# Optimization experiments

Measured on AMD Instinct MI355X. Metric: run time of the kernel, lower is better.

The kernel has to match this reference:

```python
import jax, jax.numpy as jnp
import numpy as np
from jax import lax

EPS = 1e-4
THRESHOLD = 0.0


@jax.custom_vjp
def ternary(x):
    return jnp.where(x <= -THRESHOLD, -1.0,
                     jnp.where(x >= THRESHOLD, 1.0, 0.0)).astype(x.dtype)


def _ternary_fwd(x):
    return ternary(x), x


def _ternary_bwd(x, g):
    # STE: pass gradient where -1 < x < 1, zero where |x| >= 1
    mask = (x < 1.0) & (x > -1.0)
    return (g * mask.astype(g.dtype),)


ternary.defvjp(_ternary_fwd, _ternary_bwd)


def setup_inputs() -> dict:
    key = jax.random.key(0)
    k1, k2, k3 = jax.random.split(key, 3)
    N, C_in, H, W = 32, 256, 56, 56
    C_out, K = 256, 3
    x = jax.random.normal(k1, (N, C_in, H, W), dtype=jnp.float32)
    gamma = jnp.ones((C_in,), dtype=jnp.float32)
    beta = jnp.zeros((C_in,), dtype=jnp.float32)
    fan_in = C_in * K * K
    weight = jax.random.normal(k2, (C_out, C_in, K, K), dtype=jnp.float32) / np.sqrt(fan_in)
    bias = jax.random.normal(k3, (C_out,), dtype=jnp.float32) * 0.01
    return {"x": x, "gamma": gamma, "beta": beta, "weight": weight, "bias": bias}


def reference(x, gamma, beta, weight, bias):
    # BatchNorm2d (training mode: batch statistics, biased var), eps=1e-4
    mean = jnp.mean(x, axis=(0, 2, 3), keepdims=True)
    var = jnp.mean(jnp.square(x - mean), axis=(0, 2, 3), keepdims=True)
    xn = (x - mean) * lax.rsqrt(var + EPS)
    xn = xn * gamma[None, :, None, None] + beta[None, :, None, None]
    # Ternarize to {-1, 0, 1}
    t = ternary(xn)
    # Conv2d stride=1, padding=1 (NCHW / OIHW)
    y = lax.conv_general_dilated(
        t, weight, window_strides=(1, 1), padding=[(1, 1), (1, 1)],
        dimension_numbers=("NCHW", "OIHW", "NCHW"))
    y = y + bias[None, :, None, None]
    return jax.nn.relu(y)
```

## Files before the change

### kernel.cpp

```cpp
#include <hip/hip_runtime.h>
#include <stdint.h>

#define NN 32
#define CI 256
#define CO 256
#define HH 56
#define WW 56
#define TPH 58
#define TPW 72
#define CNT (NN*HH*WW)

typedef int i32x4 __attribute__((ext_vector_type(4)));

__device__ __forceinline__ void gld16(const void* g, void* l) {
    __builtin_amdgcn_global_load_lds(
        (const __attribute__((address_space(1))) void*)(uintptr_t)g,
        (__attribute__((address_space(3))) void*)(uint32_t)(uintptr_t)l,
        16, 0, 0);
}

__global__ void stats_part(const float* __restrict__ x, double* __restrict__ part) {
    const int c = blockIdx.x, sp = blockIdx.y;
    double s = 0.0, ss = 0.0;
    const size_t base = ((size_t)(sp * 4) * CI + c) * 3136;
    for (int idx = threadIdx.x; idx < 4 * 784; idx += 256) {
        int nl = idx / 784, q = idx % 784;
        const float4 v = *(const float4*)(x + base + (size_t)nl * CI * 3136 + q * 4);
        double a = v.x, b = v.y, cc = v.z, d = v.w;
        s  += (a + b) + (cc + d);
        ss += (a * a + b * b) + (cc * cc + d * d);
    }
    for (int off = 32; off > 0; off >>= 1) {
        s  += __shfl_down(s, off, 64);
        ss += __shfl_down(ss, off, 64);
    }
    __shared__ double red[8];
    int wid = threadIdx.x >> 6, lane = threadIdx.x & 63;
    if (lane == 0) { red[wid] = s; red[4 + wid] = ss; }
    __syncthreads();
    if (threadIdx.x == 0) {
        part[(sp * 256 + c) * 2]     = (red[0] + red[1]) + (red[2] + red[3]);
        part[(sp * 256 + c) * 2 + 1] = (red[4] + red[5]) + (red[6] + red[7]);
    }
}

__global__ void wtrans_kernel(const float* __restrict__ w,
                              int8_t* __restrict__ wT,
                              float* __restrict__ qscale) {
    const int co = blockIdx.x;
    const float* wp = w + (size_t)co * 2304;
    float v[9], m = 0.f;
#pragma unroll
    for (int it = 0; it < 9; ++it) {
        v[it] = wp[threadIdx.x + it * 256];
        m = fmaxf(m, fabsf(v[it]));
    }
    for (int off = 32; off > 0; off >>= 1) m = fmaxf(m, __shfl_down(m, off, 64));
    __shared__ float red[4];
    __shared__ float qsh;
    int wid = threadIdx.x >> 6, lane = threadIdx.x & 63;
    if (lane == 0) red[wid] = m;
    __syncthreads();
    if (threadIdx.x == 0) {
        float mx = fmaxf(fmaxf(red[0], red[1]), fmaxf(red[2], red[3]));
        float q = (mx > 0.f) ? mx / 127.f : 1.f;
        qsh = q;
        qscale[co] = q;
    }
    __syncthreads();
    const float q = qsh;
#pragma unroll
    for (int it = 0; it < 9; ++it) {
        int idx = threadIdx.x + it * 256;
        int ci = idx / 9, tap = idx % 9;
        int chunk = ci >> 6, cis = ci & 63;
        int iq = __float2int_rn(v[it] / q);
        iq = iq > 127 ? 127 : (iq < -127 ? -127 : iq);
        wT[((size_t)(tap * 4 + chunk) * 256 + co) * 64 + cis] = (int8_t)iq;
    }
}

__global__ void ternarize_kernel(const float* __restrict__ x,
                                 const double* __restrict__ part,
                                 const float* __restrict__ gamma,
                                 const float* __restrict__ beta,
                                 int8_t* __restrict__ tp) {
    const int h = blockIdx.x, n = blockIdx.y;
    i32x4* rowp = (i32x4*)(tp + ((size_t)n * TPH + h) * TPW * CI);
    if (h == 0 || h == TPH - 1) {
        const i32x4 z = {0, 0, 0, 0};
        for (int p = threadIdx.x; p < TPW * 16; p += 256) rowp[p] = z;
        return;
    }
    __shared__ double Ssc[256], Ssh[256];
    {
        const int c = threadIdx.x;
        double S = 0.0, SS = 0.0;
#pragma unroll
        for (int sp = 0; sp < 8; ++sp) {
            S  += part[(sp * 256 + c) * 2];
            SS += part[(sp * 256 + c) * 2 + 1];
        }
        double mean = S / (double)CNT;
        double var  = SS / (double)CNT - mean * mean;
        double invstd = 1.0 / sqrt(var + 1e-4);
        double scale = (double)gamma[c] * invstd;
        Ssc[c] = scale;
        Ssh[c] = (double)beta[c] - mean * scale;
    }
    __shared__ int8_t L[56 * 260];
    __syncthreads();
    const int hin = h - 1;
    const size_t xb = ((size_t)n * CI) * 3136 + (size_t)hin * 56;
    for (int idx = threadIdx.x; idx < CI * 14; idx += 256) {
        int ci = idx / 14, w4 = idx - ci * 14;
        const float4 v = *(const float4*)(x + xb + (size_t)ci * 3136 + w4 * 4);
        const double sc = Ssc[ci], sh = Ssh[ci];
        const int w = w4 * 4;
        L[(w + 0) * 260 + ci] = (fma(sc, (double)v.x, sh) > 0.0) ? (int8_t)1 : (int8_t)-1;
        L[(w + 1) * 260 + ci] = (fma(sc, (double)v.y, sh) > 0.0) ? (int8_t)1 : (int8_t)-1;
        L[(w + 2) * 260 + ci] = (fma(sc, (double)v.z, sh) > 0.0) ? (int8_t)1 : (int8_t)-1;
        L[(w + 3) * 260 + ci] = (fma(sc, (double)v.w, sh) > 0.0) ? (int8_t)1 : (int8_t)-1;
    }
    __syncthreads();
    for (int p = threadIdx.x; p < TPW * 16; p += 256) {
        int wo = p >> 4, c16 = p & 15;
        i32x4 v = {0, 0, 0, 0};
        if (wo >= 1 && wo <= 56) {
            const int* lp = (const int*)&L[(wo - 1) * 260 + c16 * 16];
            v.x = lp[0]; v.y = lp[1]; v.z = lp[2]; v.w = lp[3];
        }
        rowp[p] = v;
    }
}

#define CONV_LDS (6 * TPW * 64)

__device__ __forceinline__ void stage6(const int8_t* __restrict__ g0,
                                       int8_t* lbuf, int chunk, int tid) {
#pragma unroll
    for (int j = 0; j < 7; ++j) {
        int p = tid + j * 256;
        if (j < 6 || tid < 192) {
            int row = p / 288, rem = p - row * 288;
            int wp = rem >> 2, s = rem & 3;
            int g = (s - wp) & 3;
            gld16(g0 + (size_t)row * TPW * CI + wp * 256 + chunk * 64 + g * 16,
                  lbuf + p * 16);
        }
    }
}

__launch_bounds__(256, 2)
__global__ void conv_kernel(const int8_t* __restrict__ wT,
                            const int8_t* __restrict__ tp,
                            const float* __restrict__ bias,
                            const float* __restrict__ qscale,
                            float* __restrict__ out) {
    const int co_t = blockIdx.x;
    const int h0   = blockIdx.y * 4;
    const int n    = blockIdx.z;
    const int tid  = threadIdx.x;
    const int lane = tid & 63, wid = tid >> 6;
    const int l15 = lane & 15, qd = lane >> 4;
    const int m_off = (wid & 1) * 64;
    const int rs = (wid >> 1) * 2;

    __shared__ __align__(16) int8_t Bsh[2 * CONV_LDS];

    i32x4 acc[4][4][2];
#pragma unroll
    for (int i = 0; i < 4; ++i)
#pragma unroll
        for (int j = 0; j < 4; ++j)
#pragma unroll
            for (int r = 0; r < 2; ++r) acc[i][j][r] = (i32x4){0, 0, 0, 0};

    const int8_t* g0 = tp + ((size_t)n * TPH + h0) * TPW * CI;

    stage6(g0, Bsh, 0, tid);
    for (int c = 0; c < 4; ++c) {
        __syncthreads();
        if (c < 3) stage6(g0, Bsh + ((c + 1) & 1) * CONV_LDS, c + 1, tid);
        const int8_t* lb = Bsh + (c & 1) * CONV_LDS;
#pragma unroll
        for (int kh = 0; kh < 3; ++kh) {
#pragma unroll
            for (int kw = 0; kw < 3; ++kw) {
                const int tap = kh * 3 + kw;
                const i32x4* ap = (const i32x4*)(wT +
                    ((size_t)(tap * 4 + c) * 256 + co_t * 128 + m_off) * 64);
                i32x4 a[4], b[4][2];
#pragma unroll
                for (int i = 0; i < 4; ++i)
                    a[i] = ap[(i * 16 + l15) * 4 + qd];
#pragma unroll
                for (int j = 0; j < 4; ++j) {
                    const int wp = j * 16 + l15 + kw;
                    const int slot = (qd + wp) & 3;
#pragma unroll
                    for (int r = 0; r < 2; ++r)
                        b[j][r] = *(const i32x4*)&lb[((rs + r + kh) * TPW + wp) * 64 + slot * 16];
                }
                __builtin_amdgcn_s_setprio(1);
#pragma unroll
                for (int i = 0; i < 4; ++i)
#pragma unroll
                    for (int j = 0; j < 4; ++j)
#pragma unroll
                        for (int r = 0; r < 2; ++r)
                            acc[i][j][r] = __builtin_amdgcn_mfma_i32_16x16x64_i8(
                                a[i], b[j][r], acc[i][j][r], 0, 0, 0);
                __builtin_amdgcn_s_setprio(0);
            }
        }
    }

    const int h_out = h0 + rs;
#pragma unroll
    for (int i = 0; i < 4; ++i) {
        const int co = co_t * 128 + m_off + i * 16 + qd * 4;
        const float4 bv = *(const float4*)&bias[co];
        const float4 qv = *(const float4*)&qscale[co];
        const float bb[4] = {bv.x, bv.y, bv.z, bv.w};
        const float qq[4] = {qv.x, qv.y, qv.z, qv.w};
#pragma unroll
        for (int j = 0; j < 4; ++j) {
            const int w = j * 16 + l15;
            if (w < 56) {
#pragma unroll
                for (int rr = 0; rr < 2; ++rr) {
                    const size_t ob = (((size_t)n * CO + co) * HH + (h_out + rr)) * WW + w;
#pragma unroll
                    for (int r = 0; r < 4; ++r) {
                        float v = (float)acc[i][j][rr][r] * qq[r] + bb[r];
                        out[ob + (size_t)r * (HH * WW)] = v > 0.f ? v : 0.f;
                    }
                }
            }
        }
    }
}

extern "C" void kernel_launch(void* const* d_in, const int* in_sizes, int n_in,
                              void* d_out, int out_size, void* d_ws, size_t ws_size,
                              hipStream_t stream) {
    const float* x      = (const float*)d_in[0];
    const float* gamma  = (const float*)d_in[1];
    const float* beta   = (const float*)d_in[2];
    const float* weight = (const float*)d_in[3];
    const float* bias   = (const float*)d_in[4];
    float* out = (float*)d_out;

    double* part    = (double*)d_ws;
    float*  qscale  = (float*) ((char*)d_ws + 36864);
    int8_t* wT      = (int8_t*)((char*)d_ws + 65536);
    int8_t* tp      = (int8_t*)((char*)d_ws + 1048576);

    wtrans_kernel<<<256, 256, 0, stream>>>(weight, wT, qscale);
    stats_part<<<dim3(256, 8), 256, 0, stream>>>(x, part);
    ternarize_kernel<<<dim3(TPH, NN), 256, 0, stream>>>(x, part, gamma, beta, tp);
    conv_kernel<<<dim3(2, 14, NN), 256, 0, stream>>>(wT, tp, bias, qscale, out);
}
```

Measured before the change: 316.1 us.

## Prefetch conv weight fragments, relayout LDS tile, and remap blocks across XCDs

The conv kernel now double-buffers the weight (A) fragments in registers: the next tap's weights are loaded while the current tap's MFMAs run, which hides global load latency. The LDS layout of the staged activation tile changes from a rotated 4-slot swizzle to a plane-per-16-byte-slice layout, which simplifies address math and is intended to avoid bank conflicts. The grid becomes 1D with a block index remap that spreads consecutive work across the 8 XCDs. These changes add register pressure from the second A buffer, and the new LDS layout could bring back bank conflicts.

```diff
diff --git a/kernel.cpp b/kernel.cpp
--- a/kernel.cpp
+++ b/kernel.cpp
@@ -134,7 +134,7 @@
     }
 }
 
-#define CONV_LDS (6 * TPW * 64)
+#define CONV_LDS (6 * 4 * TPW * 16)
 
 __device__ __forceinline__ void stage6(const int8_t* __restrict__ g0,
                                        int8_t* lbuf, int chunk, int tid) {
@@ -143,9 +143,8 @@
         int p = tid + j * 256;
         if (j < 6 || tid < 192) {
             int row = p / 288, rem = p - row * 288;
-            int wp = rem >> 2, s = rem & 3;
-            int g = (s - wp) & 3;
-            gld16(g0 + (size_t)row * TPW * CI + wp * 256 + chunk * 64 + g * 16,
+            int s = rem / 72, wp = rem - s * 72;
+            gld16(g0 + (size_t)row * TPW * CI + wp * 256 + chunk * 64 + s * 16,
                   lbuf + p * 16);
         }
     }
@@ -157,14 +156,19 @@
                             const float* __restrict__ bias,
                             const float* __restrict__ qscale,
                             float* __restrict__ out) {
-    const int co_t = blockIdx.x;
-    const int h0   = blockIdx.y * 4;
-    const int n    = blockIdx.z;
+    const int bid  = blockIdx.x;
+    const int lin  = (bid & 7) * 112 + (bid >> 3);
+    const int co_t = lin & 1;
+    const int yb   = (lin >> 1) % 14;
+    const int n    = lin / 28;
+    const int h0   = yb * 4;
+
     const int tid  = threadIdx.x;
     const int lane = tid & 63, wid = tid >> 6;
     const int l15 = lane & 15, qd = lane >> 4;
     const int m_off = (wid & 1) * 64;
     const int rs = (wid >> 1) * 2;
+    const int aoff = l15 * 64 + qd * 16;
 
     __shared__ __align__(16) int8_t Bsh[2 * CONV_LDS];
 
@@ -178,30 +182,40 @@
 
     const int8_t* g0 = tp + ((size_t)n * TPH + h0) * TPW * CI;
 
+#define LOADA(dst, cc_, tap_) do {                                              \
+    const int8_t* ap_ = wT +                                                    \
+        (((size_t)((tap_) * 4 + (cc_)) * 256 + co_t * 128 + m_off) << 6) + aoff;\
+    dst[0] = *(const i32x4*)(ap_);                                              \
+    dst[1] = *(const i32x4*)(ap_ + 1024);                                       \
+    dst[2] = *(const i32x4*)(ap_ + 2048);                                       \
+    dst[3] = *(const i32x4*)(ap_ + 3072);                                       \
+} while (0)
+
+    i32x4 a[2][4];
     stage6(g0, Bsh, 0, tid);
-    for (int c = 0; c < 4; ++c) {
-        __syncthreads();
-        if (c < 3) stage6(g0, Bsh + ((c + 1) & 1) * CONV_LDS, c + 1, tid);
-        const int8_t* lb = Bsh + (c & 1) * CONV_LDS;
-#pragma unroll
-        for (int kh = 0; kh < 3; ++kh) {
-#pragma unroll
-            for (int kw = 0; kw < 3; ++kw) {
-                const int tap = kh * 3 + kw;
-                const i32x4* ap = (const i32x4*)(wT +
-                    ((size_t)(tap * 4 + c) * 256 + co_t * 128 + m_off) * 64);
-                i32x4 a[4], b[4][2];
-#pragma unroll
-                for (int i = 0; i < 4; ++i)
-                    a[i] = ap[(i * 16 + l15) * 4 + qd];
+    LOADA(a[0], 0, 0);
+
+    for (int c2 = 0; c2 < 2; ++c2) {
+#pragma unroll
+        for (int cc = 0; cc < 2; ++cc) {
+            const int c = c2 * 2 + cc;
+            __syncthreads();
+            if (c < 3) stage6(g0, Bsh + (cc ^ 1) * CONV_LDS, c + 1, tid);
+            const int8_t* lb = Bsh + cc * CONV_LDS;
+#pragma unroll
+            for (int tap = 0; tap < 9; ++tap) {
+                const int kh = tap / 3, kw = tap % 3;
+                const int cur = (cc * 9 + tap) & 1, nxt = cur ^ 1;
+                i32x4 b[4][2];
 #pragma unroll
                 for (int j = 0; j < 4; ++j) {
                     const int wp = j * 16 + l15 + kw;
-                    const int slot = (qd + wp) & 3;
 #pragma unroll
                     for (int r = 0; r < 2; ++r)
-                        b[j][r] = *(const i32x4*)&lb[((rs + r + kh) * TPW + wp) * 64 + slot * 16];
+                        b[j][r] = *(const i32x4*)&lb[(((rs + r + kh) * 4 + qd) * 72 + wp) * 16];
                 }
+                if (tap < 8)      LOADA(a[nxt], c, tap + 1);
+                else if (c < 3)   LOADA(a[nxt], c + 1, 0);
                 __builtin_amdgcn_s_setprio(1);
 #pragma unroll
                 for (int i = 0; i < 4; ++i)
@@ -210,11 +224,12 @@
 #pragma unroll
                         for (int r = 0; r < 2; ++r)
                             acc[i][j][r] = __builtin_amdgcn_mfma_i32_16x16x64_i8(
-                                a[i], b[j][r], acc[i][j][r], 0, 0, 0);
+                                a[cur][i], b[j][r], acc[i][j][r], 0, 0, 0);
                 __builtin_amdgcn_s_setprio(0);
             }
         }
     }
+#undef LOADA
 
     const int h_out = h0 + rs;
 #pragma unroll
@@ -260,5 +275,5 @@
     wtrans_kernel<<<256, 256, 0, stream>>>(weight, wT, qscale);
     stats_part<<<dim3(256, 8), 256, 0, stream>>>(x, part);
     ternarize_kernel<<<dim3(TPH, NN), 256, 0, stream>>>(x, part, gamma, beta, tp);
-    conv_kernel<<<dim3(2, 14, NN), 256, 0, stream>>>(wT, tp, bias, qscale, out);
-}
+    conv_kernel<<<896, 256, 0, stream>>>(wT, tp, bias, qscale, out);
+}
```

New measurement: 328.0 us. 3.7% more time.
